# Optimization experiments

Hardware: AMD Instinct MI355X
Metric: run time of the kernel (lower is better)

## Reference

```python
import jax, jax.numpy as jnp
import numpy as np

B, T, D_ENC, H, NUM_CLASSES = 256, 256, 512, 512, 96


def setup_inputs() -> dict:
    key = jax.random.key(0)
    ks = jax.random.split(key, 12)
    s = lambda k, shp, fan: jax.random.normal(k, shp, jnp.float32) / np.sqrt(fan)
    return {
        "prev_h": jax.random.normal(ks[0], (B, H), jnp.float32),
        "prev_c": jax.random.normal(ks[1], (B, H), jnp.float32),
        "batch_H": jax.random.normal(ks[2], (B, T, D_ENC), jnp.float32),
        "char_onehots": jax.random.uniform(ks[3], (B, NUM_CLASSES), jnp.float32),
        # i2h: Dense(D_ENC -> H, no bias); h2h: Dense(H -> H, bias); score: Dense(H -> 1, no bias)
        "Wi2h": s(ks[4], (D_ENC, H), D_ENC),
        "Wh2h": s(ks[5], (H, H), H),
        "bh2h": jnp.zeros((H,), jnp.float32),
        "Wscore": s(ks[6], (H, 1), H),
        # LSTMCell: input dim = D_ENC + NUM_CLASSES, gates [i, f, g, o]
        "Wk": s(ks[7], (D_ENC + NUM_CLASSES, 4 * H), D_ENC + NUM_CLASSES),
        "Uk": s(ks[8], (H, 4 * H), H),
        "bk": jnp.zeros((4 * H,), jnp.float32),
    }


def reference(prev_h, prev_c, batch_H, char_onehots, Wi2h, Wh2h, bh2h, Wscore, Wk, Uk, bk):
    # Bahdanau additive attention
    bH_proj = jnp.einsum('btd,dh->bth', batch_H, Wi2h)          # [B,T,H]
    h_proj = (prev_h @ Wh2h + bh2h)[:, None, :]                  # [B,1,H]
    e = jnp.tanh(bH_proj + h_proj) @ Wscore                      # [B,T,1]
    alpha = jax.nn.softmax(e, axis=1)                            # [B,T,1]
    context = jnp.einsum('bt,btd->bd', alpha[..., 0], batch_H)   # [B,D_enc]
    # LSTM cell step on [context ; char_onehots]
    x = jnp.concatenate([context, char_onehots], axis=1)         # [B, D_enc+num_classes]
    z = x @ Wk + prev_h @ Uk + bk                                # [B, 4H]
    i, f, g, o = jnp.split(z, 4, axis=1)
    c_new = jax.nn.sigmoid(f) * prev_c + jax.nn.sigmoid(i) * jnp.tanh(g)
    h_new = jax.nn.sigmoid(o) * jnp.tanh(c_new)
    return h_new, c_new, alpha
```

## Files before the change

kernel.cpp:

```cpp
#include <hip/hip_runtime.h>

typedef __bf16 bf16_t;
typedef bf16_t bf16x8 __attribute__((ext_vector_type(8)));
typedef unsigned short ushort8_t __attribute__((ext_vector_type(8)));
typedef unsigned short ushort4_t __attribute__((ext_vector_type(4)));
typedef float f32x4 __attribute__((ext_vector_type(4)));

__device__ __forceinline__ unsigned short f2bf(float f) {
    union { float f; unsigned int u; } v; v.f = f;
    unsigned int r = v.u + 0x7FFFu + ((v.u >> 16) & 1u);
    return (unsigned short)(r >> 16);
}
__device__ __forceinline__ float fast_tanh(float x) {
    float e2 = __expf(2.f * x);
    return 1.f - 2.f / (e2 + 1.f);
}
__device__ __forceinline__ float fast_sig(float x) {
    return 1.f / (1.f + __expf(-x));
}

__global__ void k0_wt2(const float* __restrict__ Wi2h, const float* __restrict__ Wh2h,
                       unsigned short* __restrict__ Wt, unsigned short* __restrict__ Wht) {
    __shared__ float tile[32][33];
    const float* W = blockIdx.z ? Wh2h : Wi2h;
    unsigned short* O = blockIdx.z ? Wht : Wt;
    int tx = threadIdx.x, ty = threadIdx.y;
    int bx = blockIdx.x, by = blockIdx.y;
#pragma unroll
    for (int j = 0; j < 4; ++j) {
        int r = by * 32 + ty + j * 8;
        int c = bx * 32 + tx;
        tile[ty + j * 8][tx] = W[r * 512 + c];
    }
    __syncthreads();
#pragma unroll
    for (int j = 0; j < 4; ++j) {
        int h = bx * 32 + ty + j * 8;
        int d = by * 32 + tx;
        O[h * 512 + d] = f2bf(tile[tx][ty + j * 8]);
    }
}

__global__ void k1x_conv(const float* __restrict__ src, unsigned short* __restrict__ dst) {
    int i = blockIdx.x * 256 + threadIdx.x;
    float4 f = ((const float4*)src)[i];
    ushort4_t u;
    u[0] = f2bf(f.x); u[1] = f2bf(f.y); u[2] = f2bf(f.z); u[3] = f2bf(f.w);
    ((ushort4_t*)dst)[i] = u;
}

__global__ void k1m_hproj(const unsigned short* __restrict__ ph_bf,
                          const unsigned short* __restrict__ Wht,
                          const float* __restrict__ bh2h,
                          float* __restrict__ h_proj) {
    int tid = threadIdx.x;
    int wave = tid >> 6, lane = tid & 63;
    int l15 = lane & 15, g = lane >> 4;
    int h0 = blockIdx.x * 64 + wave * 16;
    int m0 = blockIdx.y * 32;

    f32x4 acc[2];
    acc[0] = (f32x4){0.f, 0.f, 0.f, 0.f};
    acc[1] = (f32x4){0.f, 0.f, 0.f, 0.f};

    const unsigned short* abase = ph_bf + (size_t)(m0 + l15) * 512 + g * 8;
    const unsigned short* bbase = Wht + (size_t)(h0 + l15) * 512 + g * 8;
#pragma unroll
    for (int j = 0; j < 16; ++j) {
        bf16x8 bf = __builtin_bit_cast(bf16x8, *(const ushort8_t*)(bbase + j * 32));
        bf16x8 a0 = __builtin_bit_cast(bf16x8, *(const ushort8_t*)(abase + j * 32));
        bf16x8 a1 = __builtin_bit_cast(bf16x8, *(const ushort8_t*)(abase + 16 * 512 + j * 32));
        acc[0] = __builtin_amdgcn_mfma_f32_16x16x32_bf16(a0, bf, acc[0], 0, 0, 0);
        acc[1] = __builtin_amdgcn_mfma_f32_16x16x32_bf16(a1, bf, acc[1], 0, 0, 0);
    }
    int h = h0 + l15;
    float bias = bh2h[h];
#pragma unroll
    for (int mf = 0; mf < 2; ++mf)
#pragma unroll
        for (int r = 0; r < 4; ++r)
            h_proj[(size_t)(m0 + mf * 16 + g * 4 + r) * 512 + h] = acc[mf][r] + bias;
}

__launch_bounds__(256, 2)
__global__ void k2_scores(const float* __restrict__ batch_H,
                          const unsigned short* __restrict__ Wt,
                          const float* __restrict__ h_proj,
                          const float* __restrict__ Wscore,
                          float* __restrict__ e_part) {
    __shared__ __align__(16) unsigned short Alds[8192];
    __shared__ __align__(16) unsigned short Blds[8192];
    __shared__ float hp_s[128];
    __shared__ float wsc_s[128];
    __shared__ float e_red[4][64];

    int tid = threadIdx.x;
    int wg = (blockIdx.x & 7) * 256 + (blockIdx.x >> 3);
    int mt = wg >> 2, nt = wg & 3;
    int m0 = mt * 128, n0 = nt * 128;
    int b  = m0 >> 8;

    if (tid < 128) hp_s[tid] = h_proj[(size_t)b * 512 + n0 + tid];
    else           wsc_s[tid - 128] = Wscore[n0 + tid - 128];

    int wave = tid >> 6;
    int lane = tid & 63;
    int wr = wave >> 1;
    int wc = wave & 1;
    int l15 = lane & 15, g = lane >> 4;
    int bchunk = ((lane & 7) ^ (lane >> 3)) << 3;
    int brow_l = lane >> 3;

    f32x4 acc[4][4];
#pragma unroll
    for (int mf = 0; mf < 4; ++mf)
#pragma unroll
        for (int nf = 0; nf < 4; ++nf)
            acc[mf][nf] = (f32x4){0.f, 0.f, 0.f, 0.f};

    for (int ks = 0; ks < 8; ++ks) {
        __syncthreads();
        int kbase = ks * 64;
#pragma unroll
        for (int i = 0; i < 4; ++i) {
            int q = wave * 4 + i;
            int row = q * 8 + brow_l;
            const unsigned short* gsrc = Wt + (size_t)(n0 + row) * 512 + kbase + bchunk;
            __builtin_amdgcn_global_load_lds(
                (const __attribute__((address_space(1))) void*)gsrc,
                (__attribute__((address_space(3))) void*)&Blds[q * 512], 16, 0, 0);
        }
        float4 av[8];
#pragma unroll
        for (int j = 0; j < 8; ++j) {
            int idx = j * 256 + tid;
            int r = idx >> 4, c4 = idx & 15;
            av[j] = *(const float4*)(batch_H + (size_t)(m0 + r) * 512 + kbase + c4 * 4);
        }
#pragma unroll
        for (int j = 0; j < 8; ++j) {
            int idx = j * 256 + tid;
            int r = idx >> 4, c4 = idx & 15;
            ushort4_t u;
            u[0] = f2bf(av[j].x); u[1] = f2bf(av[j].y);
            u[2] = f2bf(av[j].z); u[3] = f2bf(av[j].w);
            int boff = r * 128 + ((((c4 >> 1) ^ (r & 7)) << 4) | ((c4 & 1) << 3));
            *(ushort4_t*)((char*)Alds + boff) = u;
        }
        __syncthreads();
#pragma unroll
        for (int kk = 0; kk < 2; ++kk) {
            bf16x8 af[4], bf[4];
#pragma unroll
            for (int mf = 0; mf < 4; ++mf) {
                int row = wr * 64 + mf * 16 + l15;
                int boff = row * 128 + ((((kk * 4 + g) ^ (l15 & 7))) << 4);
                af[mf] = __builtin_bit_cast(bf16x8, *(const ushort8_t*)((char*)Alds + boff));
            }
#pragma unroll
            for (int nf = 0; nf < 4; ++nf) {
                int row = wc * 64 + nf * 16 + l15;
                int boff = row * 128 + ((((kk * 4 + g) ^ (l15 & 7))) << 4);
                bf[nf] = __builtin_bit_cast(bf16x8, *(const ushort8_t*)((char*)Blds + boff));
            }
#pragma unroll
            for (int nf = 0; nf < 4; ++nf)
#pragma unroll
                for (int mf = 0; mf < 4; ++mf)
                    acc[mf][nf] = __builtin_amdgcn_mfma_f32_16x16x32_bf16(
                        af[mf], bf[nf], acc[mf][nf], 0, 0, 0);
        }
    }

    float s[4][4];
#pragma unroll
    for (int mf = 0; mf < 4; ++mf)
#pragma unroll
        for (int r = 0; r < 4; ++r) s[mf][r] = 0.f;

#pragma unroll
    for (int nf = 0; nf < 4; ++nf) {
        int nl = wc * 64 + nf * 16 + l15;
        float hpv = hp_s[nl], wv = wsc_s[nl];
#pragma unroll
        for (int mf = 0; mf < 4; ++mf)
#pragma unroll
            for (int r = 0; r < 4; ++r)
                s[mf][r] += wv * fast_tanh(acc[mf][nf][r] + hpv);
    }
#pragma unroll
    for (int mf = 0; mf < 4; ++mf)
#pragma unroll
        for (int r = 0; r < 4; ++r) {
            float v = s[mf][r];
            v += __shfl_xor(v, 1);
            v += __shfl_xor(v, 2);
            v += __shfl_xor(v, 4);
            v += __shfl_xor(v, 8);
            s[mf][r] = v;
        }
    if (l15 == 0) {
#pragma unroll
        for (int mf = 0; mf < 4; ++mf)
#pragma unroll
            for (int r = 0; r < 4; ++r)
                e_red[wave][mf * 16 + g * 4 + r] = s[mf][r];
    }
    __syncthreads();
    if (tid < 128) {
        int wrr = tid >> 6, i64 = tid & 63;
        float v = e_red[wrr * 2 + 0][i64] + e_red[wrr * 2 + 1][i64];
        e_part[(size_t)nt * 65536 + m0 + tid] = v;
    }
}

__global__ void k3_softmax(const float* __restrict__ e_part, float* __restrict__ alpha_out) {
    __shared__ float red[4];
    int b = blockIdx.x, tid = threadIdx.x;
    int m = b * 256 + tid;
    float v = e_part[m] + e_part[65536 + m] + e_part[131072 + m] + e_part[196608 + m];
    float mx = v;
#pragma unroll
    for (int off = 32; off; off >>= 1) mx = fmaxf(mx, __shfl_xor(mx, off));
    if ((tid & 63) == 0) red[tid >> 6] = mx;
    __syncthreads();
    mx = fmaxf(fmaxf(red[0], red[1]), fmaxf(red[2], red[3]));
    float p = __expf(v - mx);
    __syncthreads();
    float sum = p;
#pragma unroll
    for (int off = 32; off; off >>= 1) sum += __shfl_xor(sum, off);
    if ((tid & 63) == 0) red[tid >> 6] = sum;
    __syncthreads();
    sum = red[0] + red[1] + red[2] + red[3];
    alpha_out[b * 256 + tid] = p / sum;
}

__global__ void k4_context(const float* __restrict__ batch_H, const float* __restrict__ alpha,
                           float* __restrict__ context) {
    __shared__ float al[256];
    int b = blockIdx.y, dc = blockIdx.x, tid = threadIdx.x;
    al[tid] = alpha[b * 256 + tid];
    __syncthreads();
    int d = dc * 256 + tid;
    const float* bh = batch_H + (size_t)b * 256 * 512 + d;
    float acc = 0.f;
#pragma unroll 4
    for (int t = 0; t < 256; ++t)
        acc += al[t] * bh[(size_t)t * 512];
    context[b * 512 + d] = acc;
}

__global__ void k5t_wzt(const float* __restrict__ Wk, const float* __restrict__ Uk,
                        unsigned short* __restrict__ Wzt) {
    __shared__ float tile[32][33];
    int tx = threadIdx.x, ty = threadIdx.y;
    int bx = blockIdx.x;
    int by = blockIdx.y;
#pragma unroll
    for (int j = 0; j < 4; ++j) {
        int k = bx * 32 + ty + j * 8;
        int c = by * 32 + tx;
        float v = (k < 608) ? Wk[(size_t)k * 2048 + c] : Uk[(size_t)(k - 608) * 2048 + c];
        tile[ty + j * 8][tx] = v;
    }
    __syncthreads();
#pragma unroll
    for (int j = 0; j < 4; ++j) {
        int n = by * 32 + ty + j * 8;
        int k = bx * 32 + tx;
        Wzt[(size_t)n * 1120 + k] = f2bf(tile[tx][ty + j * 8]);
    }
}

__global__ void k5x_build(const float* __restrict__ context, const float* __restrict__ onehots,
                          const float* __restrict__ prev_h, unsigned short* __restrict__ xb) {
    int b = blockIdx.x, tid = threadIdx.x;
    for (int k = tid; k < 1120; k += 256) {
        float v;
        if (k < 512)      v = context[b * 512 + k];
        else if (k < 608) v = onehots[b * 96 + k - 512];
        else              v = prev_h[b * 512 + k - 608];
        xb[b * 1120 + k] = f2bf(v);
    }
}

__launch_bounds__(256)
__global__ void k5m_fused(const unsigned short* __restrict__ xb,
                          const unsigned short* __restrict__ Wzt,
                          const float* __restrict__ bk,
                          const float* __restrict__ prev_c,
                          float* __restrict__ out) {
    __shared__ __align__(16) unsigned short Axs[32 * 232];

    int tid  = threadIdx.x;
    int wave = tid >> 6;
    int lane = tid & 63;
    int l15  = lane & 15;
    int g    = lane >> 4;
    int b0   = blockIdx.y * 32;
    int h0   = blockIdx.x * 64 + wave * 16;

    f32x4 acc[2][4];
#pragma unroll
    for (int mf = 0; mf < 2; ++mf)
#pragma unroll
        for (int gt = 0; gt < 4; ++gt)
            acc[mf][gt] = (f32x4){0.f, 0.f, 0.f, 0.f};

    const unsigned short* wbase = Wzt + (size_t)(h0 + l15) * 1120;

    for (int ks = 0; ks < 5; ++ks) {
        if (ks) __syncthreads();
        int kbase = ks * 224;
        for (int i = tid; i < 896; i += 256) {
            int row = i / 28;
            int c8  = (i % 28) * 8;
            *(ushort8_t*)(&Axs[row * 232 + c8]) =
                *(const ushort8_t*)(&xb[(size_t)(b0 + row) * 1120 + kbase + c8]);
        }
        __syncthreads();

        bf16x8 bcur[4], bnxt[4];
#pragma unroll
        for (int gt = 0; gt < 4; ++gt)
            bcur[gt] = __builtin_bit_cast(bf16x8,
                *(const ushort8_t*)(wbase + (size_t)gt * 512 * 1120 + kbase + g * 8));

#pragma unroll
        for (int kb = 0; kb < 7; ++kb) {
            if (kb < 6) {
                int kg = kbase + (kb + 1) * 32 + g * 8;
#pragma unroll
                for (int gt = 0; gt < 4; ++gt)
                    bnxt[gt] = __builtin_bit_cast(bf16x8,
                        *(const ushort8_t*)(wbase + (size_t)gt * 512 * 1120 + kg));
            }
            bf16x8 afrag[2];
#pragma unroll
            for (int mf = 0; mf < 2; ++mf)
                afrag[mf] = __builtin_bit_cast(bf16x8,
                    *(const ushort8_t*)(&Axs[(mf * 16 + l15) * 232 + kb * 32 + g * 8]));
#pragma unroll
            for (int gt = 0; gt < 4; ++gt)
#pragma unroll
                for (int mf = 0; mf < 2; ++mf)
                    acc[mf][gt] = __builtin_amdgcn_mfma_f32_16x16x32_bf16(
                        afrag[mf], bcur[gt], acc[mf][gt], 0, 0, 0);
#pragma unroll
            for (int gt = 0; gt < 4; ++gt) bcur[gt] = bnxt[gt];
        }
    }

    int h = h0 + l15;
    float bi = bk[h], bfv = bk[512 + h], bg = bk[1024 + h], bo = bk[1536 + h];
#pragma unroll
    for (int mf = 0; mf < 2; ++mf)
#pragma unroll
        for (int r = 0; r < 4; ++r) {
            int m = b0 + mf * 16 + g * 4 + r;
            float zi = acc[mf][0][r] + bi;
            float zf = acc[mf][1][r] + bfv;
            float zg = acc[mf][2][r] + bg;
            float zo = acc[mf][3][r] + bo;
            float c  = fast_sig(zf) * prev_c[m * 512 + h] + fast_sig(zi) * fast_tanh(zg);
            float hn = fast_sig(zo) * fast_tanh(c);
            out[m * 512 + h]          = hn;
            out[131072 + m * 512 + h] = c;
        }
}

extern "C" void kernel_launch(void* const* d_in, const int* in_sizes, int n_in,
                              void* d_out, int out_size, void* d_ws, size_t ws_size,
                              hipStream_t stream) {
    (void)in_sizes; (void)n_in; (void)out_size; (void)ws_size;
    const float* prev_h  = (const float*)d_in[0];
    const float* prev_c  = (const float*)d_in[1];
    const float* batch_H = (const float*)d_in[2];
    const float* onehots = (const float*)d_in[3];
    const float* Wi2h    = (const float*)d_in[4];
    const float* Wh2h    = (const float*)d_in[5];
    const float* bh2h    = (const float*)d_in[6];
    const float* Wscore  = (const float*)d_in[7];
    const float* Wk      = (const float*)d_in[8];
    const float* Uk      = (const float*)d_in[9];
    const float* bk      = (const float*)d_in[10];
    float* out = (float*)d_out;
    float* alpha = out + 262144;

    char* ws = (char*)d_ws;
    unsigned short* Wt     = (unsigned short*)(ws + 0);
    unsigned short* Wht    = (unsigned short*)(ws + 524288);
    unsigned short* ph_bf  = (unsigned short*)(ws + 1048576);
    float*          h_proj = (float*)(ws + 1310720);
    float*          e_part = (float*)(ws + 1835008);
    unsigned short* Wzt    = (unsigned short*)(ws + 0);
    unsigned short* xb     = (unsigned short*)(ws + 4587520);
    float*          context= (float*)(ws + 5160960);

    k0_wt2    <<<dim3(16, 16, 2), dim3(32, 8), 0, stream>>>(Wi2h, Wh2h, Wt, Wht);
    k1x_conv  <<<128, 256, 0, stream>>>(prev_h, ph_bf);
    k1m_hproj <<<dim3(8, 8), 256, 0, stream>>>(ph_bf, Wht, bh2h, h_proj);
    k2_scores <<<2048, 256, 0, stream>>>(batch_H, Wt, h_proj, Wscore, e_part);
    k3_softmax<<<256, 256, 0, stream>>>(e_part, alpha);
    k4_context<<<dim3(2, 256), 256, 0, stream>>>(batch_H, alpha, context);
    k5t_wzt   <<<dim3(35, 64), dim3(32, 8), 0, stream>>>(Wk, Uk, Wzt);
    k5x_build <<<256, 256, 0, stream>>>(context, onehots, prev_h, xb);
    k5m_fused <<<dim3(8, 8), 256, 0, stream>>>(xb, Wzt, bk, prev_c, out);
}
```

Measured before the change: 145.5 us.

## Pre-convert batch_H to bf16 once and reuse it for scores and context

Adds a pass that converts all of batch_H to bf16 in workspace. The scores GEMM then loads bf16 tiles straight into LDS via global_load_lds, and a new context kernel reads the bf16 copy and writes bf16 context directly into the LSTM input buffer. This replaces the fp32 reads of batch_H in both the scores and context stages and removes the separate context-to-xb pass. In exchange it adds a full fp32 read plus bf16 write of the 64 MB tensor, lowers context precision, and needs a large workspace, falling back to the old path if the workspace is too small.

```diff
diff --git a/kernel.cpp b/kernel.cpp
--- a/kernel.cpp
+++ b/kernel.cpp
@@ -7,9 +7,11 @@
 typedef float f32x4 __attribute__((ext_vector_type(4)));
 
 __device__ __forceinline__ unsigned short f2bf(float f) {
-    union { float f; unsigned int u; } v; v.f = f;
-    unsigned int r = v.u + 0x7FFFu + ((v.u >> 16) & 1u);
-    return (unsigned short)(r >> 16);
+    __bf16 h = (__bf16)f;
+    return __builtin_bit_cast(unsigned short, h);
+}
+__device__ __forceinline__ float bf2f(unsigned short u) {
+    union { unsigned int i; float f; } v; v.i = ((unsigned int)u) << 16; return v.f;
 }
 __device__ __forceinline__ float fast_tanh(float x) {
     float e2 = __expf(2.f * x);
@@ -80,6 +82,136 @@
 #pragma unroll
         for (int r = 0; r < 4; ++r)
             h_proj[(size_t)(m0 + mf * 16 + g * 4 + r) * 512 + h] = acc[mf][r] + bias;
+}
+
+__global__ void k2x_conv(const float* __restrict__ src, unsigned short* __restrict__ dst) {
+    int gid = blockIdx.x * 256 + threadIdx.x;
+#pragma unroll 2
+    for (int i = gid; i < 8388608; i += 4096 * 256) {
+        float4 f = ((const float4*)src)[i];
+        ushort4_t u;
+        u[0] = f2bf(f.x); u[1] = f2bf(f.y); u[2] = f2bf(f.z); u[3] = f2bf(f.w);
+        ((ushort4_t*)dst)[i] = u;
+    }
+}
+
+__launch_bounds__(256, 2)
+__global__ void k2b_scores(const unsigned short* __restrict__ bHb,
+                           const unsigned short* __restrict__ Wt,
+                           const float* __restrict__ h_proj,
+                           const float* __restrict__ Wscore,
+                           float* __restrict__ e_part) {
+    __shared__ __align__(16) unsigned short Alds[8192];
+    __shared__ __align__(16) unsigned short Blds[8192];
+    __shared__ float hp_s[128];
+    __shared__ float wsc_s[128];
+    __shared__ float e_red[4][64];
+
+    int tid = threadIdx.x;
+    int wg = (blockIdx.x & 7) * 256 + (blockIdx.x >> 3);
+    int mt = wg >> 2, nt = wg & 3;
+    int m0 = mt * 128, n0 = nt * 128;
+    int b  = m0 >> 8;
+
+    if (tid < 128) hp_s[tid] = h_proj[(size_t)b * 512 + n0 + tid];
+    else           wsc_s[tid - 128] = Wscore[n0 + tid - 128];
+
+    int wave = tid >> 6;
+    int lane = tid & 63;
+    int wr = wave >> 1;
+    int wc = wave & 1;
+    int l15 = lane & 15, g = lane >> 4;
+    int bchunk = ((lane & 7) ^ (lane >> 3)) << 3;
+    int brow_l = lane >> 3;
+
+    f32x4 acc[4][4];
+#pragma unroll
+    for (int mf = 0; mf < 4; ++mf)
+#pragma unroll
+        for (int nf = 0; nf < 4; ++nf)
+            acc[mf][nf] = (f32x4){0.f, 0.f, 0.f, 0.f};
+
+    for (int ks = 0; ks < 8; ++ks) {
+        __syncthreads();
+        int kbase = ks * 64;
+#pragma unroll
+        for (int i = 0; i < 4; ++i) {
+            int q = wave * 4 + i;
+            int row = q * 8 + brow_l;
+            const unsigned short* gA = bHb + (size_t)(m0 + row) * 512 + kbase + bchunk;
+            __builtin_amdgcn_global_load_lds(
+                (const __attribute__((address_space(1))) void*)gA,
+                (__attribute__((address_space(3))) void*)&Alds[q * 512], 16, 0, 0);
+            const unsigned short* gB = Wt + (size_t)(n0 + row) * 512 + kbase + bchunk;
+            __builtin_amdgcn_global_load_lds(
+                (const __attribute__((address_space(1))) void*)gB,
+                (__attribute__((address_space(3))) void*)&Blds[q * 512], 16, 0, 0);
+        }
+        __syncthreads();
+#pragma unroll
+        for (int kk = 0; kk < 2; ++kk) {
+            bf16x8 af[4], bf[4];
+#pragma unroll
+            for (int mf = 0; mf < 4; ++mf) {
+                int row = wr * 64 + mf * 16 + l15;
+                int boff = row * 128 + ((((kk * 4 + g) ^ (l15 & 7))) << 4);
+                af[mf] = __builtin_bit_cast(bf16x8, *(const ushort8_t*)((char*)Alds + boff));
+            }
+#pragma unroll
+            for (int nf = 0; nf < 4; ++nf) {
+                int row = wc * 64 + nf * 16 + l15;
+                int boff = row * 128 + ((((kk * 4 + g) ^ (l15 & 7))) << 4);
+                bf[nf] = __builtin_bit_cast(bf16x8, *(const ushort8_t*)((char*)Blds + boff));
+            }
+#pragma unroll
+            for (int nf = 0; nf < 4; ++nf)
+#pragma unroll
+                for (int mf = 0; mf < 4; ++mf)
+                    acc[mf][nf] = __builtin_amdgcn_mfma_f32_16x16x32_bf16(
+                        af[mf], bf[nf], acc[mf][nf], 0, 0, 0);
+        }
+    }
+
+    float s[4][4];
+#pragma unroll
+    for (int mf = 0; mf < 4; ++mf)
+#pragma unroll
+        for (int r = 0; r < 4; ++r) s[mf][r] = 0.f;
+
+#pragma unroll
+    for (int nf = 0; nf < 4; ++nf) {
+        int nl = wc * 64 + nf * 16 + l15;
+        float hpv = hp_s[nl], wv = wsc_s[nl];
+#pragma unroll
+        for (int mf = 0; mf < 4; ++mf)
+#pragma unroll
+            for (int r = 0; r < 4; ++r)
+                s[mf][r] += wv * fast_tanh(acc[mf][nf][r] + hpv);
+    }
+#pragma unroll
+    for (int mf = 0; mf < 4; ++mf)
+#pragma unroll
+        for (int r = 0; r < 4; ++r) {
+            float v = s[mf][r];
+            v += __shfl_xor(v, 1);
+            v += __shfl_xor(v, 2);
+            v += __shfl_xor(v, 4);
+            v += __shfl_xor(v, 8);
+            s[mf][r] = v;
+        }
+    if (l15 == 0) {
+#pragma unroll
+        for (int mf = 0; mf < 4; ++mf)
+#pragma unroll
+            for (int r = 0; r < 4; ++r)
+                e_red[wave][mf * 16 + g * 4 + r] = s[mf][r];
+    }
+    __syncthreads();
+    if (tid < 128) {
+        int wrr = tid >> 6, i64 = tid & 63;
+        float v = e_red[wrr * 2 + 0][i64] + e_red[wrr * 2 + 1][i64];
+        e_part[(size_t)nt * 65536 + m0 + tid] = v;
+    }
 }
 
 __launch_bounds__(256, 2)
@@ -236,6 +368,25 @@
     alpha_out[b * 256 + tid] = p / sum;
 }
 
+__global__ void k4b_context(const unsigned short* __restrict__ bHb, const float* __restrict__ alpha,
+                            unsigned short* __restrict__ xb) {
+    __shared__ float al[256];
+    int b = blockIdx.x, tid = threadIdx.x;
+    al[tid] = alpha[b * 256 + tid];
+    __syncthreads();
+    const unsigned short* bh = bHb + (size_t)b * 256 * 512 + tid * 2;
+    float a0 = 0.f, a1 = 0.f;
+#pragma unroll 4
+    for (int t = 0; t < 256; ++t) {
+        unsigned int w = *(const unsigned int*)(bh + (size_t)t * 512);
+        float av = al[t];
+        a0 += av * bf2f((unsigned short)(w & 0xffff));
+        a1 += av * bf2f((unsigned short)(w >> 16));
+    }
+    unsigned int p = (unsigned int)f2bf(a0) | ((unsigned int)f2bf(a1) << 16);
+    *(unsigned int*)(&xb[(size_t)b * 1120 + tid * 2]) = p;
+}
+
 __global__ void k4_context(const float* __restrict__ batch_H, const float* __restrict__ alpha,
                            float* __restrict__ context) {
     __shared__ float al[256];
@@ -270,6 +421,15 @@
         int n = by * 32 + ty + j * 8;
         int k = bx * 32 + tx;
         Wzt[(size_t)n * 1120 + k] = f2bf(tile[tx][ty + j * 8]);
+    }
+}
+
+__global__ void k5x2_tail(const float* __restrict__ onehots, const float* __restrict__ prev_h,
+                          unsigned short* __restrict__ xb) {
+    int b = blockIdx.x, tid = threadIdx.x;
+    for (int k = 512 + tid; k < 1120; k += 256) {
+        float v = (k < 608) ? onehots[b * 96 + k - 512] : prev_h[b * 512 + k - 608];
+        xb[(size_t)b * 1120 + k] = f2bf(v);
     }
 }
 
@@ -281,7 +441,7 @@
         if (k < 512)      v = context[b * 512 + k];
         else if (k < 608) v = onehots[b * 96 + k - 512];
         else              v = prev_h[b * 512 + k - 608];
-        xb[b * 1120 + k] = f2bf(v);
+        xb[(size_t)b * 1120 + k] = f2bf(v);
     }
 }
 
@@ -373,7 +533,7 @@
 extern "C" void kernel_launch(void* const* d_in, const int* in_sizes, int n_in,
                               void* d_out, int out_size, void* d_ws, size_t ws_size,
                               hipStream_t stream) {
-    (void)in_sizes; (void)n_in; (void)out_size; (void)ws_size;
+    (void)in_sizes; (void)n_in; (void)out_size;
     const float* prev_h  = (const float*)d_in[0];
     const float* prev_c  = (const float*)d_in[1];
     const float* batch_H = (const float*)d_in[2];
@@ -389,22 +549,45 @@
     float* alpha = out + 262144;
 
     char* ws = (char*)d_ws;
-    unsigned short* Wt     = (unsigned short*)(ws + 0);
-    unsigned short* Wht    = (unsigned short*)(ws + 524288);
-    unsigned short* ph_bf  = (unsigned short*)(ws + 1048576);
-    float*          h_proj = (float*)(ws + 1310720);
-    float*          e_part = (float*)(ws + 1835008);
-    unsigned short* Wzt    = (unsigned short*)(ws + 0);
-    unsigned short* xb     = (unsigned short*)(ws + 4587520);
-    float*          context= (float*)(ws + 5160960);
-
-    k0_wt2    <<<dim3(16, 16, 2), dim3(32, 8), 0, stream>>>(Wi2h, Wh2h, Wt, Wht);
-    k1x_conv  <<<128, 256, 0, stream>>>(prev_h, ph_bf);
-    k1m_hproj <<<dim3(8, 8), 256, 0, stream>>>(ph_bf, Wht, bh2h, h_proj);
-    k2_scores <<<2048, 256, 0, stream>>>(batch_H, Wt, h_proj, Wscore, e_part);
-    k3_softmax<<<256, 256, 0, stream>>>(e_part, alpha);
-    k4_context<<<dim3(2, 256), 256, 0, stream>>>(batch_H, alpha, context);
-    k5t_wzt   <<<dim3(35, 64), dim3(32, 8), 0, stream>>>(Wk, Uk, Wzt);
-    k5x_build <<<256, 256, 0, stream>>>(context, onehots, prev_h, xb);
-    k5m_fused <<<dim3(8, 8), 256, 0, stream>>>(xb, Wzt, bk, prev_c, out);
-}
+
+    if (ws_size >= 70565888) {
+        unsigned short* bHb   = (unsigned short*)(ws + 0);
+        unsigned short* Wt    = (unsigned short*)(ws + 67108864);
+        unsigned short* Wht   = (unsigned short*)(ws + 67633152);
+        unsigned short* ph_bf = (unsigned short*)(ws + 68157440);
+        float*          h_proj= (float*)(ws + 68419584);
+        float*          e_part= (float*)(ws + 68943872);
+        unsigned short* xb    = (unsigned short*)(ws + 69992448);
+        unsigned short* Wzt   = (unsigned short*)(ws + 0);
+
+        k0_wt2    <<<dim3(16, 16, 2), dim3(32, 8), 0, stream>>>(Wi2h, Wh2h, Wt, Wht);
+        k1x_conv  <<<128, 256, 0, stream>>>(prev_h, ph_bf);
+        k1m_hproj <<<dim3(8, 8), 256, 0, stream>>>(ph_bf, Wht, bh2h, h_proj);
+        k2x_conv  <<<4096, 256, 0, stream>>>(batch_H, bHb);
+        k2b_scores<<<2048, 256, 0, stream>>>(bHb, Wt, h_proj, Wscore, e_part);
+        k3_softmax<<<256, 256, 0, stream>>>(e_part, alpha);
+        k4b_context<<<256, 256, 0, stream>>>(bHb, alpha, xb);
+        k5x2_tail <<<256, 256, 0, stream>>>(onehots, prev_h, xb);
+        k5t_wzt   <<<dim3(35, 64), dim3(32, 8), 0, stream>>>(Wk, Uk, Wzt);
+        k5m_fused <<<dim3(8, 8), 256, 0, stream>>>(xb, Wzt, bk, prev_c, out);
+    } else {
+        unsigned short* Wt     = (unsigned short*)(ws + 0);
+        unsigned short* Wht    = (unsigned short*)(ws + 524288);
+        unsigned short* ph_bf  = (unsigned short*)(ws + 1048576);
+        float*          h_proj = (float*)(ws + 1310720);
+        float*          e_part = (float*)(ws + 1835008);
+        unsigned short* Wzt    = (unsigned short*)(ws + 0);
+        unsigned short* xb     = (unsigned short*)(ws + 4587520);
+        float*          context= (float*)(ws + 5160960);
+
+        k0_wt2    <<<dim3(16, 16, 2), dim3(32, 8), 0, stream>>>(Wi2h, Wh2h, Wt, Wht);
+        k1x_conv  <<<128, 256, 0, stream>>>(prev_h, ph_bf);
+        k1m_hproj <<<dim3(8, 8), 256, 0, stream>>>(ph_bf, Wht, bh2h, h_proj);
+        k2_scores <<<2048, 256, 0, stream>>>(batch_H, Wt, h_proj, Wscore, e_part);
+        k3_softmax<<<256, 256, 0, stream>>>(e_part, alpha);
+        k4_context<<<dim3(2, 256), 256, 0, stream>>>(batch_H, alpha, context);
+        k5t_wzt   <<<dim3(35, 64), dim3(32, 8), 0, stream>>>(Wk, Uk, Wzt);
+        k5x_build <<<256, 256, 0, stream>>>(context, onehots, prev_h, xb);
+        k5m_fused <<<dim3(8, 8), 256, 0, stream>>>(xb, Wzt, bk, prev_c, out);
+    }
+}
```

Result: slower. 162.0 us (+11.3%).

## Make score kernel hold full-K A tile in LDS and loop over all N

Applied to the files above, without the earlier changes.

Restructures the attention-score GEMM so each block converts a 128-row slice of batch_H to bf16 once, keeping the whole K=512 slice in LDS (128 KB), and then loops over all four 128-column N chunks. B fragments are read straight from global memory into registers through a 4-deep prefetch ring instead of going through LDS. Because the reduction over N now happens in-block, the partial-score buffer and the 4-way sum in the softmax go away, and batch_H is read and converted once instead of four times. The cost is one block per CU at most (large LDS), fewer blocks (512), and uncached-by-LDS global loads for the weights. The bf16 conversion also switches to the compiler cast.

```diff
diff --git a/kernel.cpp b/kernel.cpp
--- a/kernel.cpp
+++ b/kernel.cpp
@@ -7,9 +7,8 @@
 typedef float f32x4 __attribute__((ext_vector_type(4)));
 
 __device__ __forceinline__ unsigned short f2bf(float f) {
-    union { float f; unsigned int u; } v; v.f = f;
-    unsigned int r = v.u + 0x7FFFu + ((v.u >> 16) & 1u);
-    return (unsigned short)(r >> 16);
+    __bf16 h = (__bf16)f;
+    return __builtin_bit_cast(unsigned short, h);
 }
 __device__ __forceinline__ float fast_tanh(float x) {
     float e2 = __expf(2.f * x);
@@ -82,112 +81,111 @@
             h_proj[(size_t)(m0 + mf * 16 + g * 4 + r) * 512 + h] = acc[mf][r] + bias;
 }
 
-__launch_bounds__(256, 2)
-__global__ void k2_scores(const float* __restrict__ batch_H,
-                          const unsigned short* __restrict__ Wt,
-                          const float* __restrict__ h_proj,
-                          const float* __restrict__ Wscore,
-                          float* __restrict__ e_part) {
-    __shared__ __align__(16) unsigned short Alds[8192];
-    __shared__ __align__(16) unsigned short Blds[8192];
-    __shared__ float hp_s[128];
-    __shared__ float wsc_s[128];
+__launch_bounds__(256, 1)
+__global__ void k2v4_scores(const float* __restrict__ batch_H,
+                            const unsigned short* __restrict__ Wt,
+                            const float* __restrict__ h_proj,
+                            const float* __restrict__ Wscore,
+                            float* __restrict__ e_out) {
+    __shared__ __align__(16) unsigned short Asw[128 * 512];
+    __shared__ float hp_s[512];
+    __shared__ float wsc_s[512];
     __shared__ float e_red[4][64];
 
     int tid = threadIdx.x;
-    int wg = (blockIdx.x & 7) * 256 + (blockIdx.x >> 3);
-    int mt = wg >> 2, nt = wg & 3;
-    int m0 = mt * 128, n0 = nt * 128;
-    int b  = m0 >> 8;
-
-    if (tid < 128) hp_s[tid] = h_proj[(size_t)b * 512 + n0 + tid];
-    else           wsc_s[tid - 128] = Wscore[n0 + tid - 128];
+    int m0  = blockIdx.x * 128;
+    int b   = m0 >> 8;
+
+    hp_s[tid]        = h_proj[(size_t)b * 512 + tid];
+    hp_s[tid + 256]  = h_proj[(size_t)b * 512 + tid + 256];
+    wsc_s[tid]       = Wscore[tid];
+    wsc_s[tid + 256] = Wscore[tid + 256];
+
+    {
+        int dr = tid >> 4;
+        int cc = tid & 15;
+#pragma unroll
+        for (int j = 0; j < 32; ++j) {
+            int r = (j >> 2) * 16 + dr;
+            int c = (j & 3) * 16 + cc;
+            const float* src = batch_H + (size_t)(m0 + r) * 512 + c * 8;
+            float4 f0 = *(const float4*)(src);
+            float4 f1 = *(const float4*)(src + 4);
+            ushort8_t u;
+            u[0] = f2bf(f0.x); u[1] = f2bf(f0.y); u[2] = f2bf(f0.z); u[3] = f2bf(f0.w);
+            u[4] = f2bf(f1.x); u[5] = f2bf(f1.y); u[6] = f2bf(f1.z); u[7] = f2bf(f1.w);
+            *(ushort8_t*)((char*)Asw + r * 1024 + ((c ^ (r & 7)) << 4)) = u;
+        }
+    }
+    __syncthreads();
 
     int wave = tid >> 6;
     int lane = tid & 63;
     int wr = wave >> 1;
     int wc = wave & 1;
     int l15 = lane & 15, g = lane >> 4;
-    int bchunk = ((lane & 7) ^ (lane >> 3)) << 3;
-    int brow_l = lane >> 3;
-
-    f32x4 acc[4][4];
+
+    float s[4][4];
 #pragma unroll
     for (int mf = 0; mf < 4; ++mf)
 #pragma unroll
-        for (int nf = 0; nf < 4; ++nf)
-            acc[mf][nf] = (f32x4){0.f, 0.f, 0.f, 0.f};
-
-    for (int ks = 0; ks < 8; ++ks) {
-        __syncthreads();
-        int kbase = ks * 64;
-#pragma unroll
-        for (int i = 0; i < 4; ++i) {
-            int q = wave * 4 + i;
-            int row = q * 8 + brow_l;
-            const unsigned short* gsrc = Wt + (size_t)(n0 + row) * 512 + kbase + bchunk;
-            __builtin_amdgcn_global_load_lds(
-                (const __attribute__((address_space(1))) void*)gsrc,
-                (__attribute__((address_space(3))) void*)&Blds[q * 512], 16, 0, 0);
-        }
-        float4 av[8];
-#pragma unroll
-        for (int j = 0; j < 8; ++j) {
-            int idx = j * 256 + tid;
-            int r = idx >> 4, c4 = idx & 15;
-            av[j] = *(const float4*)(batch_H + (size_t)(m0 + r) * 512 + kbase + c4 * 4);
-        }
-#pragma unroll
-        for (int j = 0; j < 8; ++j) {
-            int idx = j * 256 + tid;
-            int r = idx >> 4, c4 = idx & 15;
-            ushort4_t u;
-            u[0] = f2bf(av[j].x); u[1] = f2bf(av[j].y);
-            u[2] = f2bf(av[j].z); u[3] = f2bf(av[j].w);
-            int boff = r * 128 + ((((c4 >> 1) ^ (r & 7)) << 4) | ((c4 & 1) << 3));
-            *(ushort4_t*)((char*)Alds + boff) = u;
-        }
-        __syncthreads();
-#pragma unroll
-        for (int kk = 0; kk < 2; ++kk) {
-            bf16x8 af[4], bf[4];
+        for (int r = 0; r < 4; ++r) s[mf][r] = 0.f;
+
+    const unsigned short* wtb = Wt + (size_t)(wc * 64 + l15) * 512 + g * 8;
+
+    for (int nc = 0; nc < 4; ++nc) {
+        f32x4 acc[4][4];
+#pragma unroll
+        for (int mf = 0; mf < 4; ++mf)
+#pragma unroll
+            for (int nf = 0; nf < 4; ++nf)
+                acc[mf][nf] = (f32x4){0.f, 0.f, 0.f, 0.f};
+
+        const unsigned short* wnc = wtb + (size_t)nc * 128 * 512;
+
+        bf16x8 bq[4][4];
+#pragma unroll
+        for (int ks0 = 0; ks0 < 4; ++ks0)
+#pragma unroll
+            for (int nf = 0; nf < 4; ++nf)
+                bq[ks0][nf] = __builtin_bit_cast(bf16x8,
+                    *(const ushort8_t*)(wnc + (size_t)nf * 16 * 512 + ks0 * 32));
+
+#pragma unroll
+        for (int ks = 0; ks < 16; ++ks) {
+            bf16x8 af[4];
 #pragma unroll
             for (int mf = 0; mf < 4; ++mf) {
                 int row = wr * 64 + mf * 16 + l15;
-                int boff = row * 128 + ((((kk * 4 + g) ^ (l15 & 7))) << 4);
-                af[mf] = __builtin_bit_cast(bf16x8, *(const ushort8_t*)((char*)Alds + boff));
-            }
-#pragma unroll
-            for (int nf = 0; nf < 4; ++nf) {
-                int row = wc * 64 + nf * 16 + l15;
-                int boff = row * 128 + ((((kk * 4 + g) ^ (l15 & 7))) << 4);
-                bf[nf] = __builtin_bit_cast(bf16x8, *(const ushort8_t*)((char*)Blds + boff));
+                af[mf] = __builtin_bit_cast(bf16x8,
+                    *(const ushort8_t*)((char*)Asw + row * 1024 + (((ks * 4 + g) ^ (row & 7)) << 4)));
             }
 #pragma unroll
             for (int nf = 0; nf < 4; ++nf)
 #pragma unroll
                 for (int mf = 0; mf < 4; ++mf)
                     acc[mf][nf] = __builtin_amdgcn_mfma_f32_16x16x32_bf16(
-                        af[mf], bf[nf], acc[mf][nf], 0, 0, 0);
-        }
-    }
-
-    float s[4][4];
-#pragma unroll
-    for (int mf = 0; mf < 4; ++mf)
-#pragma unroll
-        for (int r = 0; r < 4; ++r) s[mf][r] = 0.f;
-
-#pragma unroll
-    for (int nf = 0; nf < 4; ++nf) {
-        int nl = wc * 64 + nf * 16 + l15;
-        float hpv = hp_s[nl], wv = wsc_s[nl];
-#pragma unroll
-        for (int mf = 0; mf < 4; ++mf)
-#pragma unroll
-            for (int r = 0; r < 4; ++r)
-                s[mf][r] += wv * fast_tanh(acc[mf][nf][r] + hpv);
-    }
+                        af[mf], bq[ks & 3][nf], acc[mf][nf], 0, 0, 0);
+            if (ks < 12) {
+#pragma unroll
+                for (int nf = 0; nf < 4; ++nf)
+                    bq[ks & 3][nf] = __builtin_bit_cast(bf16x8,
+                        *(const ushort8_t*)(wnc + (size_t)nf * 16 * 512 + (ks + 4) * 32));
+            }
+        }
+
+#pragma unroll
+        for (int nf = 0; nf < 4; ++nf) {
+            int nl = nc * 128 + wc * 64 + nf * 16 + l15;
+            float hpv = hp_s[nl], wv = wsc_s[nl];
+#pragma unroll
+            for (int mf = 0; mf < 4; ++mf)
+#pragma unroll
+                for (int r = 0; r < 4; ++r)
+                    s[mf][r] += wv * fast_tanh(acc[mf][nf][r] + hpv);
+        }
+    }
+
 #pragma unroll
     for (int mf = 0; mf < 4; ++mf)
 #pragma unroll
@@ -208,17 +206,15 @@
     }
     __syncthreads();
     if (tid < 128) {
-        int wrr = tid >> 6, i64 = tid & 63;
-        float v = e_red[wrr * 2 + 0][i64] + e_red[wrr * 2 + 1][i64];
-        e_part[(size_t)nt * 65536 + m0 + tid] = v;
-    }
-}
-
-__global__ void k3_softmax(const float* __restrict__ e_part, float* __restrict__ alpha_out) {
+        int wrr = tid >> 6, rl = tid & 63;
+        e_out[m0 + wrr * 64 + rl] = e_red[wrr * 2 + 0][rl] + e_red[wrr * 2 + 1][rl];
+    }
+}
+
+__global__ void k3_softmax(const float* __restrict__ e, float* __restrict__ alpha_out) {
     __shared__ float red[4];
     int b = blockIdx.x, tid = threadIdx.x;
-    int m = b * 256 + tid;
-    float v = e_part[m] + e_part[65536 + m] + e_part[131072 + m] + e_part[196608 + m];
+    float v = e[b * 256 + tid];
     float mx = v;
 #pragma unroll
     for (int off = 32; off; off >>= 1) mx = fmaxf(mx, __shfl_xor(mx, off));
@@ -281,7 +277,7 @@
         if (k < 512)      v = context[b * 512 + k];
         else if (k < 608) v = onehots[b * 96 + k - 512];
         else              v = prev_h[b * 512 + k - 608];
-        xb[b * 1120 + k] = f2bf(v);
+        xb[(size_t)b * 1120 + k] = f2bf(v);
     }
 }
 
@@ -393,18 +389,18 @@
     unsigned short* Wht    = (unsigned short*)(ws + 524288);
     unsigned short* ph_bf  = (unsigned short*)(ws + 1048576);
     float*          h_proj = (float*)(ws + 1310720);
-    float*          e_part = (float*)(ws + 1835008);
+    float*          e      = (float*)(ws + 1835008);
     unsigned short* Wzt    = (unsigned short*)(ws + 0);
     unsigned short* xb     = (unsigned short*)(ws + 4587520);
     float*          context= (float*)(ws + 5160960);
 
-    k0_wt2    <<<dim3(16, 16, 2), dim3(32, 8), 0, stream>>>(Wi2h, Wh2h, Wt, Wht);
-    k1x_conv  <<<128, 256, 0, stream>>>(prev_h, ph_bf);
-    k1m_hproj <<<dim3(8, 8), 256, 0, stream>>>(ph_bf, Wht, bh2h, h_proj);
-    k2_scores <<<2048, 256, 0, stream>>>(batch_H, Wt, h_proj, Wscore, e_part);
-    k3_softmax<<<256, 256, 0, stream>>>(e_part, alpha);
-    k4_context<<<dim3(2, 256), 256, 0, stream>>>(batch_H, alpha, context);
-    k5t_wzt   <<<dim3(35, 64), dim3(32, 8), 0, stream>>>(Wk, Uk, Wzt);
-    k5x_build <<<256, 256, 0, stream>>>(context, onehots, prev_h, xb);
-    k5m_fused <<<dim3(8, 8), 256, 0, stream>>>(xb, Wzt, bk, prev_c, out);
-}
+    k0_wt2     <<<dim3(16, 16, 2), dim3(32, 8), 0, stream>>>(Wi2h, Wh2h, Wt, Wht);
+    k1x_conv   <<<128, 256, 0, stream>>>(prev_h, ph_bf);
+    k1m_hproj  <<<dim3(8, 8), 256, 0, stream>>>(ph_bf, Wht, bh2h, h_proj);
+    k2v4_scores<<<512, 256, 0, stream>>>(batch_H, Wt, h_proj, Wscore, e);
+    k3_softmax <<<256, 256, 0, stream>>>(e, alpha);
+    k4_context <<<dim3(2, 256), 256, 0, stream>>>(batch_H, alpha, context);
+    k5t_wzt    <<<dim3(35, 64), dim3(32, 8), 0, stream>>>(Wk, Uk, Wzt);
+    k5x_build  <<<256, 256, 0, stream>>>(context, onehots, prev_h, xb);
+    k5m_fused  <<<dim3(8, 8), 256, 0, stream>>>(xb, Wzt, bk, prev_c, out);
+}
```

New measurement: 177.5 us. 22.0% more time.
